# Optimization experiments

Measured on AMD Instinct MI355X. Metric: run time of the kernel, lower is better.

Reference implementation:

```python
import jax, jax.numpy as jnp
import numpy as np

N = 20000      # nodes
E = 640000     # edges
H = 128        # hidden_channels
F = 128        # num_filters
G = 50         # num_gaussians
L = 6          # num_interactions
CUT = 10.0     # cutoff
NG = 64        # num graphs in batch
NODE_CLASS = 100


def ssp(x):
    # ShiftedSoftplus: softplus(x) - log(2)
    return jax.nn.softplus(x) - jnp.asarray(np.log(2.0), x.dtype)


def setup_inputs() -> dict:
    key = jax.random.key(0)
    ks = jax.random.split(key, 20)
    z = jax.random.randint(ks[0], (N,), 0, NODE_CLASS)
    pos = jax.random.normal(ks[1], (N, 3), dtype=jnp.float32) * 3.0
    edge_index = jax.random.randint(ks[2], (2, E), 0, N)
    batch = jnp.sort(jax.random.randint(ks[3], (N,), 0, NG))
    s = 0.05
    emb = jax.random.normal(ks[4], (NODE_CLASS, H), dtype=jnp.float32) * s
    mlp_w1 = jax.random.normal(ks[5], (L, G, F), dtype=jnp.float32) * s
    mlp_b1 = jnp.zeros((L, F), jnp.float32)
    mlp_w2 = jax.random.normal(ks[6], (L, F, F), dtype=jnp.float32) * s
    mlp_b2 = jnp.zeros((L, F), jnp.float32)
    conv_w1 = jax.random.normal(ks[7], (L, H, F), dtype=jnp.float32) * s
    conv_w2 = jax.random.normal(ks[8], (L, F, H), dtype=jnp.float32) * s
    conv_b2 = jnp.zeros((L, H), jnp.float32)
    lin_w = jax.random.normal(ks[9], (L, H, H), dtype=jnp.float32) * s
    lin_b = jnp.zeros((L, H), jnp.float32)
    out1_w = jax.random.normal(ks[10], (H, H), dtype=jnp.float32) * s
    out1_b = jnp.zeros((H,), jnp.float32)
    out2_w = jax.random.normal(ks[11], (H, H), dtype=jnp.float32) * s
    out2_b = jnp.zeros((H,), jnp.float32)
    return dict(z=z, pos=pos, edge_index=edge_index, batch=batch, emb=emb,
                mlp_w1=mlp_w1, mlp_b1=mlp_b1, mlp_w2=mlp_w2, mlp_b2=mlp_b2,
                conv_w1=conv_w1, conv_w2=conv_w2, conv_b2=conv_b2,
                lin_w=lin_w, lin_b=lin_b,
                out1_w=out1_w, out1_b=out1_b, out2_w=out2_w, out2_b=out2_b)


def reference(z, pos, edge_index, batch, emb,
              mlp_w1, mlp_b1, mlp_w2, mlp_b2,
              conv_w1, conv_w2, conv_b2, lin_w, lin_b,
              out1_w, out1_b, out2_w, out2_b):
    src, dst = edge_index[0], edge_index[1]  # x_j = x[src], aggregate at dst
    h = emb[z]                               # [N, H]
    d = jnp.linalg.norm(pos[src] - pos[dst], axis=-1)  # [E]
    # GaussianSmearing(0, cutoff, G)
    offset = jnp.linspace(0.0, CUT, G).astype(d.dtype)
    coeff = -0.5 / (offset[1] - offset[0]) ** 2
    edge_attr = jnp.exp(coeff * (d[:, None] - offset[None, :]) ** 2)  # [E, G]
    # cosine cutoff
    C = 0.5 * (jnp.cos(d * jnp.pi / CUT) + 1.0)  # [E]
    n = h.shape[0]
    for l in range(L):
        # edge filter: mlp(edge_attr) * C
        W = ssp(edge_attr @ mlp_w1[l] + mlp_b1[l]) @ mlp_w2[l] + mlp_b2[l]
        W = W * C[:, None]                      # [E, F]
        xf = h @ conv_w1[l]                     # lin1, no bias: [N, F]
        msg = xf[src] * W                       # gather + weight
        agg = jax.ops.segment_sum(msg, dst, num_segments=n)  # scatter-add
        x = agg @ conv_w2[l] + conv_b2[l]       # lin2
        x = ssp(x)
        x = x @ lin_w[l] + lin_b[l]
        h = h + x                               # residual
    h = ssp(h @ out1_w + out1_b) @ out2_w + out2_b
    # readout = 'mean'
    sums = jax.ops.segment_sum(h, batch, num_segments=NG)
    cnt = jax.ops.segment_sum(jnp.ones((n,), h.dtype), batch, num_segments=NG)
    return sums / jnp.maximum(cnt, 1.0)[:, None]
```

## Files before the change

### kernel.cpp

```cpp
#include <hip/hip_runtime.h>
#include <math.h>

#define NN 20000
#define NE 640000
#define GDIM 50
#define LAYERS 6
#define NGRAPH 64
#define TBL 2048
#define DMAXF 12.8f
#define G2_PAD 136

typedef __attribute__((ext_vector_type(8))) short short8;
typedef __attribute__((ext_vector_type(4))) float floatx4;

__device__ __forceinline__ float sspf(float x) {
    float sp = (x > 30.0f) ? x : log1pf(expf(x));
    return sp - 0.69314718055994530942f;
}

__device__ __forceinline__ unsigned short f2bs(float f) {
    union { float f; unsigned int i; } u; u.f = f;
    unsigned int r = u.i + 0x7fffu + ((u.i >> 16) & 1u);
    return (unsigned short)(r >> 16);
}

__device__ __forceinline__ float bs2f(unsigned int bits16) {
    union { unsigned int i; float f; } u; u.i = bits16 << 16;
    return u.f;
}

__device__ __forceinline__ short8 pack_bf16x8(float4 a, float4 b) {
    short8 o;
    o[0] = (short)f2bs(a.x); o[1] = (short)f2bs(a.y);
    o[2] = (short)f2bs(a.z); o[3] = (short)f2bs(a.w);
    o[4] = (short)f2bs(b.x); o[5] = (short)f2bs(b.y);
    o[6] = (short)f2bs(b.z); o[7] = (short)f2bs(b.w);
    return o;
}

struct WArgs { const float* s[26]; unsigned short* d[26]; };
#define PREP_WBLK 416
__global__ void prep_a(WArgs a, int* __restrict__ deg,
                       float* __restrict__ A_tab, const int* __restrict__ z,
                       const float* __restrict__ emb, float* __restrict__ h) {
    __shared__ float tile[32][33];
    int b = blockIdx.x;
    if (b < PREP_WBLK) {
        int mz = b >> 4, sub = b & 15;
        int bx = (sub & 3) * 32, by = (sub >> 2) * 32;
        const float* Wm = a.s[mz];
        unsigned short* Wo = a.d[mz];
        int tx = threadIdx.x & 31, ty = threadIdx.x >> 5;
        for (int r = ty; r < 32; r += 8) tile[r][tx] = Wm[(by + r) * 128 + bx + tx];
        __syncthreads();
        for (int r = ty; r < 32; r += 8) Wo[(bx + r) * 128 + by + tx] = f2bs(tile[tx][r]);
        return;
    }
    int idx = (b - PREP_WBLK) * 256 + threadIdx.x;
    if (idx < NN) { deg[idx] = 0; return; }
    idx -= NN;
    if (idx < (TBL + 2) * GDIM) {
        int i = idx / GDIM, g = idx % GDIM;
        float v = 0.0f;
        if (i <= TBL) {
            float d = (float)i * (DMAXF / (float)TBL);
            float step = 10.0f / 49.0f;
            float off = (float)g * step;
            float coeff = -0.5f / (step * step);
            float dd = d - off;
            v = expf(coeff * dd * dd);
        }
        A_tab[idx] = v;
        return;
    }
    idx -= (TBL + 2) * GDIM;
    if (idx < NN * 32) {
        int n = idx >> 5, q = idx & 31;
        ((float4*)h)[n * 32 + q] = ((const float4*)emb)[(size_t)z[n] * 32 + q];
    }
}

__global__ void deg_hist(const int* __restrict__ dst, int* __restrict__ deg) {
    int j = blockIdx.x * blockDim.x + threadIdx.x;
    if (j >= NE) return;
    atomicAdd(&deg[dst[j]], 1);
}

__global__ void scan_a(const int* __restrict__ deg, int* __restrict__ row_ptr,
                       int* __restrict__ bsum) {
    __shared__ int sh[256];
    int b = blockIdx.x, t = threadIdx.x;
    int i = b * 256 + t;
    int v = (i < NN) ? deg[i] : 0;
    int x = v;
    sh[t] = x;
    __syncthreads();
    for (int off = 1; off < 256; off <<= 1) {
        int u = (t >= off) ? sh[t - off] : 0;
        __syncthreads();
        x += u;
        sh[t] = x;
        __syncthreads();
    }
    if (i <= NN) row_ptr[i] = x - v;
    if (t == 255) bsum[b] = x;
}

__global__ void scan_b(const int* __restrict__ bsum, int* __restrict__ row_ptr,
                       int* __restrict__ cursor) {
    __shared__ int spref;
    int b = blockIdx.x, t = threadIdx.x;
    if (t < 64) {
        int s = 0;
        if (t < b) s += bsum[t];
        if (t + 64 < b) s += bsum[t + 64];
        for (int off = 32; off; off >>= 1) s += __shfl_down(s, off);
        if (t == 0) spref = s;
    }
    __syncthreads();
    int prefix = spref;
    int i = b * 256 + t;
    if (i < NN) {
        int v = row_ptr[i] + prefix;
        row_ptr[i] = v;
        cursor[i] = v;
    }
    if (b == 0 && t == 0) row_ptr[NN] = NE;
}

__global__ void csr_fill(const float* __restrict__ pos, const int* __restrict__ src,
                         const int* __restrict__ dst, int* __restrict__ cursor,
                         int2* __restrict__ csr) {
    int j = blockIdx.x * blockDim.x + threadIdx.x;
    if (j >= NE) return;
    int s = src[j], tno = dst[j];
    float dx = pos[3*s+0] - pos[3*tno+0];
    float dy = pos[3*s+1] - pos[3*tno+1];
    float dz = pos[3*s+2] - pos[3*tno+2];
    float d = sqrtf(dx*dx + dy*dy + dz*dz);
    float u = d * ((float)TBL / DMAXF);
    u = fminf(u, (float)(TBL + 1));
    int i0 = (int)u; if (i0 > TBL) i0 = TBL;
    float f = u - (float)i0;
    int p = atomicAdd(&cursor[tno], 1);
    csr[p] = make_int2((i0 << 15) | s, __float_as_int(f));
}

template <int K>
__launch_bounds__(256, 2)
__global__ void gemm_t(const float* __restrict__ A, const float* __restrict__ W,
                       const float* __restrict__ bias, float* __restrict__ Y, int M,
                       int act, int aStride, int wStride, int bStride, int yStride) {
    constexpr int KP = (K + 3) & ~3;
    __shared__ __align__(16) float Ws[KP * 128];
    __shared__ __align__(16) float As[32 * KP];
    int l = blockIdx.y;
    A += (size_t)l * aStride;
    W += (size_t)l * wStride;
    if (bias) bias += (size_t)l * bStride;
    Y += (size_t)l * yStride;
    int t = threadIdx.x;
    int row0 = blockIdx.x * 32;
    for (int i = t; i < KP * 128; i += 256) Ws[i] = (i < K * 128) ? W[i] : 0.0f;
    for (int i = t; i < 32 * KP; i += 256) {
        int r = i / KP, k = i % KP;
        float v = 0.f;
        if (k < K && row0 + r < M) v = A[(size_t)(row0 + r) * K + k];
        As[r * KP + k] = v;
    }
    __syncthreads();
    int tx = t & 31, ty = t >> 5;
    int c0 = tx * 4, r0 = ty * 4;
    float acc[4][4] = {{0.f}};
    #pragma unroll 4
    for (int k = 0; k < KP; k += 4) {
        float4 a0 = *(const float4*)&As[(r0 + 0) * KP + k];
        float4 a1 = *(const float4*)&As[(r0 + 1) * KP + k];
        float4 a2 = *(const float4*)&As[(r0 + 2) * KP + k];
        float4 a3 = *(const float4*)&As[(r0 + 3) * KP + k];
        float4 w0 = *(const float4*)&Ws[(k + 0) * 128 + c0];
        float4 w1 = *(const float4*)&Ws[(k + 1) * 128 + c0];
        float4 w2 = *(const float4*)&Ws[(k + 2) * 128 + c0];
        float4 w3 = *(const float4*)&Ws[(k + 3) * 128 + c0];
        float av[4][4] = {{a0.x,a0.y,a0.z,a0.w},{a1.x,a1.y,a1.z,a1.w},
                          {a2.x,a2.y,a2.z,a2.w},{a3.x,a3.y,a3.z,a3.w}};
        float wv[4][4] = {{w0.x,w0.y,w0.z,w0.w},{w1.x,w1.y,w1.z,w1.w},
                          {w2.x,w2.y,w2.z,w2.w},{w3.x,w3.y,w3.z,w3.w}};
        #pragma unroll
        for (int i = 0; i < 4; i++)
            #pragma unroll
            for (int j = 0; j < 4; j++)
                #pragma unroll
                for (int q = 0; q < 4; q++)
                    acc[i][j] += av[i][q] * wv[q][j];
    }
    float b0 = 0.f, b1 = 0.f, b2 = 0.f, b3 = 0.f;
    if (bias) { b0 = bias[c0]; b1 = bias[c0+1]; b2 = bias[c0+2]; b3 = bias[c0+3]; }
    #pragma unroll
    for (int i = 0; i < 4; i++) {
        int r = row0 + r0 + i;
        if (r >= M) break;
        float4 v;
        v.x = acc[i][0] + b0; v.y = acc[i][1] + b1; v.z = acc[i][2] + b2; v.w = acc[i][3] + b3;
        if (act == 1) { v.x = sspf(v.x); v.y = sspf(v.y); v.z = sspf(v.z); v.w = sspf(v.w); }
        *(float4*)&Y[(size_t)r * 128 + c0] = v;
    }
}

__launch_bounds__(256)
__global__ void gemm_cs2(const float* __restrict__ A1, const unsigned short* __restrict__ W1t,
                         const float* __restrict__ bias1, float* __restrict__ Y1, int M1,
                         const float* __restrict__ A2, const unsigned short* __restrict__ W2t,
                         unsigned short* __restrict__ Yb2, int M2) {
    int y = blockIdx.y;
    const float* A; const unsigned short* Wt; const float* bias;
    float* Yf; unsigned short* Yb; int M;
    if (y < LAYERS) {
        M = M1;
        A = A1 + (size_t)y * M1 * 128;
        Wt = W1t + (size_t)y * 16384;
        bias = bias1 + (size_t)y * 128;
        Yf = Y1 + (size_t)y * M1 * 128;
        Yb = nullptr;
    } else {
        M = M2; A = A2; Wt = W2t; bias = nullptr; Yf = nullptr; Yb = Yb2;
    }
    int wv = threadIdx.x >> 6, lane = threadIdx.x & 63;
    int row0 = blockIdx.x * 32;
    if (row0 >= M) return;
    int lm = lane & 15, lk = (lane >> 4) * 8, orow = (lane >> 4) * 4;
    int r0 = row0 + lm;      r0 = (r0 < M) ? r0 : M - 1;
    int r1 = row0 + 16 + lm; r1 = (r1 < M) ? r1 : M - 1;
    const float* Ap0 = A + (size_t)r0 * 128;
    const float* Ap1 = A + (size_t)r1 * 128;
    short8 af0[4], af1[4];
    #pragma unroll
    for (int kq = 0; kq < 4; kq++) {
        af0[kq] = pack_bf16x8(*(const float4*)(Ap0 + kq * 32 + lk),
                              *(const float4*)(Ap0 + kq * 32 + lk + 4));
        af1[kq] = pack_bf16x8(*(const float4*)(Ap1 + kq * 32 + lk),
                              *(const float4*)(Ap1 + kq * 32 + lk + 4));
    }
    floatx4 acc[2][2];
    #pragma unroll
    for (int i = 0; i < 2; i++)
        #pragma unroll
        for (int j = 0; j < 2; j++) acc[i][j] = (floatx4){0, 0, 0, 0};
    const unsigned short* Wp = Wt + (size_t)(wv * 32) * 128;
    #pragma unroll
    for (int kq = 0; kq < 4; kq++) {
        #pragma unroll
        for (int ct = 0; ct < 2; ct++) {
            short8 bf = *(const short8*)(Wp + (size_t)(ct * 16 + lm) * 128 + kq * 32 + lk);
            acc[0][ct] = __builtin_amdgcn_mfma_f32_16x16x32_bf16(af0[kq], bf, acc[0][ct], 0, 0, 0);
            acc[1][ct] = __builtin_amdgcn_mfma_f32_16x16x32_bf16(af1[kq], bf, acc[1][ct], 0, 0, 0);
        }
    }
    #pragma unroll
    for (int tt = 0; tt < 2; tt++) {
        #pragma unroll
        for (int ct = 0; ct < 2; ct++) {
            int c = wv * 32 + ct * 16 + lm;
            float b = bias ? bias[c] : 0.f;
            #pragma unroll
            for (int r = 0; r < 4; r++) {
                int rr = row0 + tt * 16 + orow + r;
                if (rr >= M) continue;
                float v = acc[tt][ct][r] + b;
                if (Yf) Yf[(size_t)rr * 128 + c] = v;
                if (Yb) Yb[(size_t)rr * 128 + c] = f2bs(v);
            }
        }
    }
}

__launch_bounds__(256)
__global__ void gemm3(const unsigned short* __restrict__ aggb,
                      const unsigned short* __restrict__ W2t, const float* __restrict__ b2,
                      const unsigned short* __restrict__ W3t, const float* __restrict__ b3,
                      const float* __restrict__ resid, float* __restrict__ Yf,
                      const unsigned short* __restrict__ W1nt, unsigned short* __restrict__ xfb) {
    __shared__ unsigned short Ls[16 * G2_PAD];
    int wv = threadIdx.x >> 6, lane = threadIdx.x & 63;
    int row0 = blockIdx.x * 16;
    int lm = lane & 15, lk = (lane >> 4) * 8, orow = (lane >> 4) * 4;
    int cw = wv * 32;
    float rpre[2][4];
    #pragma unroll
    for (int ct = 0; ct < 2; ct++)
        #pragma unroll
        for (int r = 0; r < 4; r++)
            rpre[ct][r] = resid[(size_t)(row0 + orow + r) * 128 + cw + ct * 16 + lm];
    {
        const unsigned short* Ap = aggb + (size_t)(row0 + lm) * 128;
        short8 af[4];
        #pragma unroll
        for (int kq = 0; kq < 4; kq++)
            af[kq] = *(const short8*)(Ap + kq * 32 + lk);
        floatx4 acc[2];
        acc[0] = (floatx4){0, 0, 0, 0}; acc[1] = (floatx4){0, 0, 0, 0};
        const unsigned short* Wp = W2t + (size_t)cw * 128;
        #pragma unroll
        for (int kq = 0; kq < 4; kq++) {
            #pragma unroll
            for (int ct = 0; ct < 2; ct++) {
                short8 bf = *(const short8*)(Wp + (size_t)(ct * 16 + lm) * 128 + kq * 32 + lk);
                acc[ct] = __builtin_amdgcn_mfma_f32_16x16x32_bf16(af[kq], bf, acc[ct], 0, 0, 0);
            }
        }
        #pragma unroll
        for (int ct = 0; ct < 2; ct++) {
            int c = cw + ct * 16 + lm;
            float b = b2[c];
            #pragma unroll
            for (int r = 0; r < 4; r++)
                Ls[(orow + r) * G2_PAD + c] = f2bs(sspf(acc[ct][r] + b));
        }
    }
    __syncthreads();
    float vout[2][4];
    {
        short8 a2[4];
        #pragma unroll
        for (int kq = 0; kq < 4; kq++)
            a2[kq] = *(const short8*)&Ls[lm * G2_PAD + kq * 32 + lk];
        floatx4 acc[2];
        acc[0] = (floatx4){0, 0, 0, 0}; acc[1] = (floatx4){0, 0, 0, 0};
        const unsigned short* Wp = W3t + (size_t)cw * 128;
        #pragma unroll
        for (int kq = 0; kq < 4; kq++) {
            #pragma unroll
            for (int ct = 0; ct < 2; ct++) {
                short8 bf = *(const short8*)(Wp + (size_t)(ct * 16 + lm) * 128 + kq * 32 + lk);
                acc[ct] = __builtin_amdgcn_mfma_f32_16x16x32_bf16(a2[kq], bf, acc[ct], 0, 0, 0);
            }
        }
        #pragma unroll
        for (int ct = 0; ct < 2; ct++) {
            int c = cw + ct * 16 + lm;
            float b = b3[c];
            #pragma unroll
            for (int r = 0; r < 4; r++) {
                int rr = row0 + orow + r;
                float v = acc[ct][r] + b + rpre[ct][r];
                Yf[(size_t)rr * 128 + c] = v;
                vout[ct][r] = v;
            }
        }
    }
    if (!W1nt) return;
    __syncthreads();
    #pragma unroll
    for (int ct = 0; ct < 2; ct++) {
        int c = cw + ct * 16 + lm;
        #pragma unroll
        for (int r = 0; r < 4; r++)
            Ls[(orow + r) * G2_PAD + c] = f2bs(vout[ct][r]);
    }
    __syncthreads();
    {
        short8 a3[4];
        #pragma unroll
        for (int kq = 0; kq < 4; kq++)
            a3[kq] = *(const short8*)&Ls[lm * G2_PAD + kq * 32 + lk];
        floatx4 acc[2];
        acc[0] = (floatx4){0, 0, 0, 0}; acc[1] = (floatx4){0, 0, 0, 0};
        const unsigned short* Wp = W1nt + (size_t)cw * 128;
        #pragma unroll
        for (int kq = 0; kq < 4; kq++) {
            #pragma unroll
            for (int ct = 0; ct < 2; ct++) {
                short8 bf = *(const short8*)(Wp + (size_t)(ct * 16 + lm) * 128 + kq * 32 + lk);
                acc[ct] = __builtin_amdgcn_mfma_f32_16x16x32_bf16(a3[kq], bf, acc[ct], 0, 0, 0);
            }
        }
        #pragma unroll
        for (int ct = 0; ct < 2; ct++) {
            int c = cw + ct * 16 + lm;
            #pragma unroll
            for (int r = 0; r < 4; r++)
                xfb[(size_t)(row0 + orow + r) * 128 + c] = f2bs(acc[ct][r]);
        }
    }
}

__launch_bounds__(256)
__global__ void gemm3h(const float* __restrict__ A,
                       const unsigned short* __restrict__ W2t, const float* __restrict__ b2,
                       const unsigned short* __restrict__ W3t, const float* __restrict__ b3,
                       float* __restrict__ Yf) {
    __shared__ unsigned short Ls[16 * G2_PAD];
    int wv = threadIdx.x >> 6, lane = threadIdx.x & 63;
    int row0 = blockIdx.x * 16;
    int lm = lane & 15, lk = (lane >> 4) * 8, orow = (lane >> 4) * 4;
    int cw = wv * 32;
    {
        const float* Ap = A + (size_t)(row0 + lm) * 128;
        short8 af[4];
        #pragma unroll
        for (int kq = 0; kq < 4; kq++)
            af[kq] = pack_bf16x8(*(const float4*)(Ap + kq * 32 + lk),
                                 *(const float4*)(Ap + kq * 32 + lk + 4));
        floatx4 acc[2];
        acc[0] = (floatx4){0, 0, 0, 0}; acc[1] = (floatx4){0, 0, 0, 0};
        const unsigned short* Wp = W2t + (size_t)cw * 128;
        #pragma unroll
        for (int kq = 0; kq < 4; kq++) {
            #pragma unroll
            for (int ct = 0; ct < 2; ct++) {
                short8 bf = *(const short8*)(Wp + (size_t)(ct * 16 + lm) * 128 + kq * 32 + lk);
                acc[ct] = __builtin_amdgcn_mfma_f32_16x16x32_bf16(af[kq], bf, acc[ct], 0, 0, 0);
            }
        }
        #pragma unroll
        for (int ct = 0; ct < 2; ct++) {
            int c = cw + ct * 16 + lm;
            float b = b2[c];
            #pragma unroll
            for (int r = 0; r < 4; r++)
                Ls[(orow + r) * G2_PAD + c] = f2bs(sspf(acc[ct][r] + b));
        }
    }
    __syncthreads();
    {
        short8 a2[4];
        #pragma unroll
        for (int kq = 0; kq < 4; kq++)
            a2[kq] = *(const short8*)&Ls[lm * G2_PAD + kq * 32 + lk];
        floatx4 acc[2];
        acc[0] = (floatx4){0, 0, 0, 0}; acc[1] = (floatx4){0, 0, 0, 0};
        const unsigned short* Wp = W3t + (size_t)cw * 128;
        #pragma unroll
        for (int kq = 0; kq < 4; kq++) {
            #pragma unroll
            for (int ct = 0; ct < 2; ct++) {
                short8 bf = *(const short8*)(Wp + (size_t)(ct * 16 + lm) * 128 + kq * 32 + lk);
                acc[ct] = __builtin_amdgcn_mfma_f32_16x16x32_bf16(a2[kq], bf, acc[ct], 0, 0, 0);
            }
        }
        #pragma unroll
        for (int ct = 0; ct < 2; ct++) {
            int c = cw + ct * 16 + lm;
            float b = b3[c];
            #pragma unroll
            for (int r = 0; r < 4; r++)
                Yf[(size_t)(row0 + orow + r) * 128 + c] = acc[ct][r] + b;
        }
    }
}

__global__ void tquant(const float* __restrict__ T, unsigned int* __restrict__ Tb) {
    int idx = blockIdx.x * blockDim.x + threadIdx.x;
    const int total = LAYERS * (TBL + 1) * 128;
    if (idx >= total) return;
    int c = idx & 127;
    int li = idx >> 7;
    int i = li % (TBL + 1);
    int l = li / (TBL + 1);
    float d0 = (float)i * (DMAXF / (float)TBL);
    float d1 = (float)(i + 1) * (DMAXF / (float)TBL);
    float C0 = 0.5f * (cosf(d0 * 0.31415926535897931f) + 1.0f);
    float C1 = 0.5f * (cosf(d1 * 0.31415926535897931f) + 1.0f);
    const float* row = T + ((size_t)l * (TBL + 2) + i) * 128 + c;
    float w = row[0] * C0;
    float nw = row[128] * C1;
    Tb[idx] = ((unsigned)f2bs(nw - w) << 16) | f2bs(w);
}

__launch_bounds__(256)
__global__ void edge_agg(const int* __restrict__ row_ptr, const int2* __restrict__ csr,
                         const unsigned int* __restrict__ Tb,
                         const unsigned short* __restrict__ xfb,
                         unsigned short* __restrict__ aggb) {
    __shared__ float red[128];
    int wv = __builtin_amdgcn_readfirstlane(threadIdx.x >> 6);
    int lane = threadIdx.x & 63;
    int n = blockIdx.x;
    int c = (wv & 1) * 64 + lane;
    int par = wv >> 1;
    int e0 = row_ptr[n], e1 = row_ptr[n + 1];
    float ax = 0.f;
    int e = e0 + par;
    for (; e + 14 < e1; e += 16) {
        unsigned int px[8]; float ff[8];
        #pragma unroll
        for (int q = 0; q < 8; q++) {
            int2 ed = csr[e + 2 * q];
            px[q] = (unsigned int)__builtin_amdgcn_readfirstlane(ed.x);
            ff[q] = __int_as_float(__builtin_amdgcn_readfirstlane(ed.y));
        }
        unsigned int tw[8]; unsigned short xv[8];
        #pragma unroll
        for (int q = 0; q < 8; q++) {
            tw[q] = Tb[(px[q] >> 15) * 128 + c];
            xv[q] = xfb[(size_t)(px[q] & 0x7fffu) * 128 + c];
        }
        #pragma unroll
        for (int q = 0; q < 8; q++) {
            float w = bs2f(tw[q] & 0xffffu), dw = bs2f(tw[q] >> 16);
            float x = bs2f((unsigned int)xv[q]);
            ax = fmaf(x, fmaf(ff[q], dw, w), ax);
        }
    }
    for (; e < e1; e += 2) {
        int2 ed = csr[e];
        unsigned int px = (unsigned int)__builtin_amdgcn_readfirstlane(ed.x);
        float f = __int_as_float(__builtin_amdgcn_readfirstlane(ed.y));
        unsigned int tw = Tb[(px >> 15) * 128 + c];
        unsigned short xv = xfb[(size_t)(px & 0x7fffu) * 128 + c];
        float w = bs2f(tw & 0xffffu), dw = bs2f(tw >> 16);
        float x = bs2f((unsigned int)xv);
        ax = fmaf(x, fmaf(f, dw, w), ax);
    }
    if (par == 1) red[c] = ax;
    __syncthreads();
    if (par == 0) aggb[(size_t)n * 128 + c] = f2bs(ax + red[c]);
}

__global__ void readout(const float* __restrict__ hout, const int* __restrict__ batch,
                        float* __restrict__ out) {
    int g = blockIdx.x;
    int t = threadIdx.x;
    int c = t & 127, half = t >> 7;
    __shared__ int sh[2];
    __shared__ float red[128];
    if (t < 2) {
        int target = g + t;
        int lo = 0, hi = NN;
        while (lo < hi) {
            int mid = (lo + hi) >> 1;
            if (batch[mid] < target) lo = mid + 1; else hi = mid;
        }
        sh[t] = lo;
    }
    __syncthreads();
    int lo = sh[0], hi = sh[1];
    float s = 0.f;
    for (int n = lo + half; n < hi; n += 2) s += hout[(size_t)n * 128 + c];
    if (half == 1) red[c] = s;
    __syncthreads();
    if (half == 0) {
        int cnt = hi - lo;
        out[g * 128 + c] = (s + red[c]) / (float)(cnt > 0 ? cnt : 1);
    }
}

extern "C" void kernel_launch(void* const* d_in, const int* in_sizes, int n_in,
                              void* d_out, int out_size, void* d_ws, size_t ws_size,
                              hipStream_t stream) {
    const int*   z       = (const int*)d_in[0];
    const float* pos     = (const float*)d_in[1];
    const int*   eidx    = (const int*)d_in[2];
    const int*   src     = eidx;
    const int*   dst     = eidx + NE;
    const int*   batch   = (const int*)d_in[3];
    const float* emb     = (const float*)d_in[4];
    const float* mlp_w1  = (const float*)d_in[5];
    const float* mlp_b1  = (const float*)d_in[6];
    const float* mlp_w2  = (const float*)d_in[7];
    const float* mlp_b2  = (const float*)d_in[8];
    const float* conv_w1 = (const float*)d_in[9];
    const float* conv_w2 = (const float*)d_in[10];
    const float* conv_b2 = (const float*)d_in[11];
    const float* lin_w   = (const float*)d_in[12];
    const float* lin_b   = (const float*)d_in[13];
    const float* out1_w  = (const float*)d_in[14];
    const float* out1_b  = (const float*)d_in[15];
    const float* out2_w  = (const float*)d_in[16];
    const float* out2_b  = (const float*)d_in[17];
    float* out = (float*)d_out;

    char* wp = (char*)d_ws;
    auto alloc = [&](size_t bytes) {
        char* p = wp;
        wp += (bytes + 255) & ~(size_t)255;
        return p;
    };
    const int Mt = TBL + 2;
    int*    deg     = (int*)alloc(NN * 4);
    int*    row_ptr = (int*)alloc((NN + 1) * 4);
    int*    cursor  = (int*)alloc(NN * 4);
    int*    bsum    = (int*)alloc(128 * 4);
    int2*   csr     = (int2*)alloc((size_t)NE * 8);
    float*  A_tab   = (float*)alloc((size_t)Mt * GDIM * 4);
    float*  T1all   = (float*)alloc((size_t)LAYERS * Mt * 128 * 4);
    float*  T       = (float*)alloc((size_t)LAYERS * Mt * 128 * 4);
    unsigned int* Tb = (unsigned int*)alloc((size_t)LAYERS * (TBL + 1) * 128 * 4);
    float*  h       = (float*)alloc((size_t)NN * 128 * 4);
    float*  hout    = (float*)alloc((size_t)NN * 128 * 4);
    unsigned short* aggb = (unsigned short*)alloc((size_t)NN * 128 * 2);
    unsigned short* xfb  = (unsigned short*)alloc((size_t)NN * 128 * 2);
    unsigned short* wbf  = (unsigned short*)alloc((size_t)26 * 16384 * 2);
    unsigned short* mlp_w2t  = wbf;
    unsigned short* conv_w1t = wbf + (size_t)6 * 16384;
    unsigned short* conv_w2t = wbf + (size_t)12 * 16384;
    unsigned short* lin_wt   = wbf + (size_t)18 * 16384;
    unsigned short* out1_wt  = wbf + (size_t)24 * 16384;
    unsigned short* out2_wt  = wbf + (size_t)25 * 16384;

    WArgs wa;
    for (int l = 0; l < 6; l++) {
        wa.s[l]      = mlp_w2  + (size_t)l * 16384;  wa.d[l]      = mlp_w2t  + (size_t)l * 16384;
        wa.s[6 + l]  = conv_w1 + (size_t)l * 16384;  wa.d[6 + l]  = conv_w1t + (size_t)l * 16384;
        wa.s[12 + l] = conv_w2 + (size_t)l * 16384;  wa.d[12 + l] = conv_w2t + (size_t)l * 16384;
        wa.s[18 + l] = lin_w   + (size_t)l * 16384;  wa.d[18 + l] = lin_wt   + (size_t)l * 16384;
    }
    wa.s[24] = out1_w; wa.d[24] = out1_wt;
    wa.s[25] = out2_w; wa.d[25] = out2_wt;
    const int initN = NN + Mt * GDIM + NN * 32;
    prep_a<<<PREP_WBLK + (initN + 255) / 256, 256, 0, stream>>>(wa, deg, A_tab, z, emb, h);

    deg_hist<<<(NE + 255) / 256, 256, 0, stream>>>(dst, deg);
    const int NB = (NN + 255) / 256;
    scan_a<<<NB, 256, 0, stream>>>(deg, row_ptr, bsum);
    scan_b<<<NB, 256, 0, stream>>>(bsum, row_ptr, cursor);
    csr_fill<<<(NE + 255) / 256, 256, 0, stream>>>(pos, src, dst, cursor, csr);

    const int gt32 = (Mt + 31) / 32;
    gemm_t<GDIM><<<dim3(gt32, LAYERS), 256, 0, stream>>>(
        A_tab, mlp_w1, mlp_b1, T1all, Mt, 1, 0, GDIM * 128, 128, Mt * 128);
    gemm_cs2<<<dim3(NN / 32, LAYERS + 1), 256, 0, stream>>>(
        T1all, mlp_w2t, mlp_b2, T, Mt,
        h, conv_w1t, xfb, NN);
    tquant<<<(LAYERS * (TBL + 1) * 128 + 255) / 256, 256, 0, stream>>>(T, Tb);

    const int gn = NN / 16;
    for (int l = 0; l < LAYERS; l++) {
        edge_agg<<<NN, 256, 0, stream>>>(row_ptr, csr,
                                         Tb + (size_t)l * (TBL + 1) * 128, xfb, aggb);
        const unsigned short* w1n = (l + 1 < LAYERS) ? conv_w1t + (size_t)(l + 1) * 16384 : nullptr;
        gemm3<<<gn, 256, 0, stream>>>(aggb, conv_w2t + (size_t)l * 16384, conv_b2 + l * 128,
                                      lin_wt + (size_t)l * 16384, lin_b + l * 128,
                                      h, h, w1n, xfb);
    }

    gemm3h<<<gn, 256, 0, stream>>>(h, out1_wt, out1_b, out2_wt, out2_b, hout);
    readout<<<NGRAPH, 256, 0, stream>>>(hout, batch, out);
}
```

Measured before the change: 632.4 us.

## Software-pipeline edge aggregation per node and fuse mean readout into output GEMM

```diff
diff --git a/kernel.cpp b/kernel.cpp
--- a/kernel.cpp
+++ b/kernel.cpp
@@ -9,6 +9,7 @@
 #define TBL 2048
 #define DMAXF 12.8f
 #define G2_PAD 136
+#define CK 8
 
 typedef __attribute__((ext_vector_type(8))) short short8;
 typedef __attribute__((ext_vector_type(4))) float floatx4;
@@ -40,9 +41,10 @@
 
 struct WArgs { const float* s[26]; unsigned short* d[26]; };
 #define PREP_WBLK 416
-__global__ void prep_a(WArgs a, int* __restrict__ deg,
+__global__ void prep_a(WArgs a, int* __restrict__ deg, float* __restrict__ out,
                        float* __restrict__ A_tab, const int* __restrict__ z,
-                       const float* __restrict__ emb, float* __restrict__ h) {
+                       const float* __restrict__ emb, float* __restrict__ h,
+                       const int* __restrict__ batch, float* __restrict__ inv_cnt) {
     __shared__ float tile[32][33];
     int b = blockIdx.x;
     if (b < PREP_WBLK) {
@@ -59,6 +61,8 @@
     int idx = (b - PREP_WBLK) * 256 + threadIdx.x;
     if (idx < NN) { deg[idx] = 0; return; }
     idx -= NN;
+    if (idx < NGRAPH * 128) { out[idx] = 0.f; return; }
+    idx -= NGRAPH * 128;
     if (idx < (TBL + 2) * GDIM) {
         int i = idx / GDIM, g = idx % GDIM;
         float v = 0.0f;
@@ -77,6 +81,16 @@
     if (idx < NN * 32) {
         int n = idx >> 5, q = idx & 31;
         ((float4*)h)[n * 32 + q] = ((const float4*)emb)[(size_t)z[n] * 32 + q];
+        return;
+    }
+    idx -= NN * 32;
+    if (idx < NGRAPH) {
+        int lo = 0, hi = NN;
+        while (lo < hi) { int m = (lo + hi) >> 1; if (batch[m] < idx) lo = m + 1; else hi = m; }
+        int lo2 = lo, hi2 = NN;
+        while (lo2 < hi2) { int m = (lo2 + hi2) >> 1; if (batch[m] < idx + 1) lo2 = m + 1; else hi2 = m; }
+        int cnt = lo2 - lo;
+        inv_cnt[idx] = 1.0f / (float)(cnt > 0 ? cnt : 1);
     }
 }
 
@@ -388,7 +402,8 @@
 __global__ void gemm3h(const float* __restrict__ A,
                        const unsigned short* __restrict__ W2t, const float* __restrict__ b2,
                        const unsigned short* __restrict__ W3t, const float* __restrict__ b3,
-                       float* __restrict__ Yf) {
+                       const int* __restrict__ batch, const float* __restrict__ inv_cnt,
+                       float* __restrict__ out) {
     __shared__ unsigned short Ls[16 * G2_PAD];
     int wv = threadIdx.x >> 6, lane = threadIdx.x & 63;
     int row0 = blockIdx.x * 16;
@@ -422,6 +437,7 @@
         }
     }
     __syncthreads();
+    float vout[2][4];
     {
         short8 a2[4];
         #pragma unroll
@@ -444,7 +460,30 @@
             float b = b3[c];
             #pragma unroll
             for (int r = 0; r < 4; r++)
-                Yf[(size_t)(row0 + orow + r) * 128 + c] = acc[ct][r] + b;
+                vout[ct][r] = acc[ct][r] + b;
+        }
+    }
+    int g0  = __builtin_amdgcn_readfirstlane(batch[row0]);
+    int g15 = __builtin_amdgcn_readfirstlane(batch[row0 + 15]);
+    if (g0 == g15) {
+        float inv = inv_cnt[g0];
+        #pragma unroll
+        for (int ct = 0; ct < 2; ct++) {
+            float s = vout[ct][0] + vout[ct][1] + vout[ct][2] + vout[ct][3];
+            s += __shfl_xor(s, 16);
+            s += __shfl_xor(s, 32);
+            if (lane < 16)
+                atomicAdd(&out[g0 * 128 + cw + ct * 16 + lm], s * inv);
+        }
+    } else {
+        #pragma unroll
+        for (int ct = 0; ct < 2; ct++) {
+            int c = cw + ct * 16 + lm;
+            #pragma unroll
+            for (int r = 0; r < 4; r++) {
+                int g = batch[row0 + orow + r];
+                atomicAdd(&out[g * 128 + c], vout[ct][r] * inv_cnt[g]);
+            }
         }
     }
 }
@@ -472,77 +511,71 @@
                          const unsigned int* __restrict__ Tb,
                          const unsigned short* __restrict__ xfb,
                          unsigned short* __restrict__ aggb) {
-    __shared__ float red[128];
     int wv = __builtin_amdgcn_readfirstlane(threadIdx.x >> 6);
     int lane = threadIdx.x & 63;
-    int n = blockIdx.x;
+    int n = blockIdx.x * 2 + (wv >> 1);
     int c = (wv & 1) * 64 + lane;
-    int par = wv >> 1;
     int e0 = row_ptr[n], e1 = row_ptr[n + 1];
     float ax = 0.f;
-    int e = e0 + par;
-    for (; e + 14 < e1; e += 16) {
-        unsigned int px[8]; float ff[8];
-        #pragma unroll
-        for (int q = 0; q < 8; q++) {
-            int2 ed = csr[e + 2 * q];
-            px[q] = (unsigned int)__builtin_amdgcn_readfirstlane(ed.x);
+
+    unsigned pxA[CK], pxB[CK];
+    float ffA[CK], ffB[CK];
+    unsigned twA[CK], twB[CK];
+    unsigned short xvA[CK], xvB[CK];
+
+    auto loadS = [&](unsigned* px, float* ff, int base) {
+        #pragma unroll
+        for (int q = 0; q < CK; q++) {
+            int2 ed = csr[base + q];
+            px[q] = (unsigned)__builtin_amdgcn_readfirstlane(ed.x);
             ff[q] = __int_as_float(__builtin_amdgcn_readfirstlane(ed.y));
         }
-        unsigned int tw[8]; unsigned short xv[8];
-        #pragma unroll
-        for (int q = 0; q < 8; q++) {
+    };
+    auto loadV = [&](unsigned* tw, unsigned short* xv, const unsigned* px) {
+        #pragma unroll
+        for (int q = 0; q < CK; q++) {
             tw[q] = Tb[(px[q] >> 15) * 128 + c];
             xv[q] = xfb[(size_t)(px[q] & 0x7fffu) * 128 + c];
         }
-        #pragma unroll
-        for (int q = 0; q < 8; q++) {
+    };
+    auto fmaC = [&](const unsigned* tw, const unsigned short* xv, const float* ff) {
+        #pragma unroll
+        for (int q = 0; q < CK; q++) {
             float w = bs2f(tw[q] & 0xffffu), dw = bs2f(tw[q] >> 16);
-            float x = bs2f((unsigned int)xv[q]);
+            float x = bs2f((unsigned)xv[q]);
             ax = fmaf(x, fmaf(ff[q], dw, w), ax);
         }
-    }
-    for (; e < e1; e += 2) {
+    };
+
+    int nfull = (e1 - e0) / CK;
+    if (nfull > 0) {
+        loadS(pxA, ffA, e0);
+        loadV(twA, xvA, pxA);
+        if (nfull > 1) loadS(pxB, ffB, e0 + CK);
+        int it = 0;
+        for (; it + 2 <= nfull; it += 2) {
+            loadV(twB, xvB, pxB);
+            fmaC(twA, xvA, ffA);
+            if (it + 2 < nfull) {
+                loadS(pxA, ffA, e0 + (it + 2) * CK);
+                loadV(twA, xvA, pxA);
+            }
+            fmaC(twB, xvB, ffB);
+            if (it + 3 < nfull) loadS(pxB, ffB, e0 + (it + 3) * CK);
+        }
+        if (it < nfull) fmaC(twA, xvA, ffA);
+    }
+    for (int e = e0 + nfull * CK; e < e1; e++) {
         int2 ed = csr[e];
-        unsigned int px = (unsigned int)__builtin_amdgcn_readfirstlane(ed.x);
+        unsigned px = (unsigned)__builtin_amdgcn_readfirstlane(ed.x);
         float f = __int_as_float(__builtin_amdgcn_readfirstlane(ed.y));
-        unsigned int tw = Tb[(px >> 15) * 128 + c];
+        unsigned tw = Tb[(px >> 15) * 128 + c];
         unsigned short xv = xfb[(size_t)(px & 0x7fffu) * 128 + c];
         float w = bs2f(tw & 0xffffu), dw = bs2f(tw >> 16);
-        float x = bs2f((unsigned int)xv);
+        float x = bs2f((unsigned)xv);
         ax = fmaf(x, fmaf(f, dw, w), ax);
     }
-    if (par == 1) red[c] = ax;
-    __syncthreads();
-    if (par == 0) aggb[(size_t)n * 128 + c] = f2bs(ax + red[c]);
-}
-
-__global__ void readout(const float* __restrict__ hout, const int* __restrict__ batch,
-                        float* __restrict__ out) {
-    int g = blockIdx.x;
-    int t = threadIdx.x;
-    int c = t & 127, half = t >> 7;
-    __shared__ int sh[2];
-    __shared__ float red[128];
-    if (t < 2) {
-        int target = g + t;
-        int lo = 0, hi = NN;
-        while (lo < hi) {
-            int mid = (lo + hi) >> 1;
-            if (batch[mid] < target) lo = mid + 1; else hi = mid;
-        }
-        sh[t] = lo;
-    }
-    __syncthreads();
-    int lo = sh[0], hi = sh[1];
-    float s = 0.f;
-    for (int n = lo + half; n < hi; n += 2) s += hout[(size_t)n * 128 + c];
-    if (half == 1) red[c] = s;
-    __syncthreads();
-    if (half == 0) {
-        int cnt = hi - lo;
-        out[g * 128 + c] = (s + red[c]) / (float)(cnt > 0 ? cnt : 1);
-    }
+    aggb[(size_t)n * 128 + c] = f2bs(ax);
 }
 
 extern "C" void kernel_launch(void* const* d_in, const int* in_sizes, int n_in,
@@ -581,13 +614,13 @@
     int*    row_ptr = (int*)alloc((NN + 1) * 4);
     int*    cursor  = (int*)alloc(NN * 4);
     int*    bsum    = (int*)alloc(128 * 4);
+    float*  inv_cnt = (float*)alloc(NGRAPH * 4);
     int2*   csr     = (int2*)alloc((size_t)NE * 8);
     float*  A_tab   = (float*)alloc((size_t)Mt * GDIM * 4);
     float*  T1all   = (float*)alloc((size_t)LAYERS * Mt * 128 * 4);
     float*  T       = (float*)alloc((size_t)LAYERS * Mt * 128 * 4);
     unsigned int* Tb = (unsigned int*)alloc((size_t)LAYERS * (TBL + 1) * 128 * 4);
     float*  h       = (float*)alloc((size_t)NN * 128 * 4);
-    float*  hout    = (float*)alloc((size_t)NN * 128 * 4);
     unsigned short* aggb = (unsigned short*)alloc((size_t)NN * 128 * 2);
     unsigned short* xfb  = (unsigned short*)alloc((size_t)NN * 128 * 2);
     unsigned short* wbf  = (unsigned short*)alloc((size_t)26 * 16384 * 2);
@@ -607,8 +640,9 @@
     }
     wa.s[24] = out1_w; wa.d[24] = out1_wt;
     wa.s[25] = out2_w; wa.d[25] = out2_wt;
-    const int initN = NN + Mt * GDIM + NN * 32;
-    prep_a<<<PREP_WBLK + (initN + 255) / 256, 256, 0, stream>>>(wa, deg, A_tab, z, emb, h);
+    const int initN = NN + NGRAPH * 128 + Mt * GDIM + NN * 32 + NGRAPH;
+    prep_a<<<PREP_WBLK + (initN + 255) / 256, 256, 0, stream>>>(wa, deg, out, A_tab, z,
+                                                                emb, h, batch, inv_cnt);
 
     deg_hist<<<(NE + 255) / 256, 256, 0, stream>>>(dst, deg);
     const int NB = (NN + 255) / 256;
@@ -626,14 +660,14 @@
 
     const int gn = NN / 16;
     for (int l = 0; l < LAYERS; l++) {
-        edge_agg<<<NN, 256, 0, stream>>>(row_ptr, csr,
-                                         Tb + (size_t)l * (TBL + 1) * 128, xfb, aggb);
+        edge_agg<<<NN / 2, 256, 0, stream>>>(row_ptr, csr,
+                                             Tb + (size_t)l * (TBL + 1) * 128, xfb, aggb);
         const unsigned short* w1n = (l + 1 < LAYERS) ? conv_w1t + (size_t)(l + 1) * 16384 : nullptr;
         gemm3<<<gn, 256, 0, stream>>>(aggb, conv_w2t + (size_t)l * 16384, conv_b2 + l * 128,
                                       lin_wt + (size_t)l * 16384, lin_b + l * 128,
                                       h, h, w1n, xfb);
     }
 
-    gemm3h<<<gn, 256, 0, stream>>>(h, out1_wt, out1_b, out2_wt, out2_b, hout);
-    readout<<<NGRAPH, 256, 0, stream>>>(hout, batch, out);
-}
+    gemm3h<<<gn, 256, 0, stream>>>(h, out1_wt, out1_b, out2_wt, out2_b,
+                                   batch, inv_cnt, out);
+}
```

New measurement: 556.5 us. -12.0%, faster.
